# Optimization experiments

Hardware: AMD Instinct MI355X
Metric: run time of the kernel (lower is better)

The kernel has to match this reference:

```python
import jax, jax.numpy as jnp
import numpy as np

B, N, K, D = 256, 64, 12, 128


def setup_inputs() -> dict:
    key = jax.random.key(0)
    ks = jax.random.split(key, 12)
    s = 1.0 / np.sqrt(D)
    inp = {
        "nodes_hidden": jax.random.normal(ks[0], (B, N, D), jnp.float32),
        "neighbors_hidden": jax.random.normal(ks[1], (B, N, K, D), jnp.float32),
        # binary neighbor-validity mask (float, as in the torch code)
        "mask": (jax.random.uniform(ks[2], (B, N, K)) < 0.7).astype(jnp.float32),
        "Wq": jax.random.uniform(ks[3], (D, D), jnp.float32, -s, s),
        "bq": jax.random.uniform(ks[4], (D,), jnp.float32, -s, s),
        "Wk": jax.random.uniform(ks[5], (D, D), jnp.float32, -s, s),
        "bk": jax.random.uniform(ks[6], (D,), jnp.float32, -s, s),
        "Wv": jax.random.uniform(ks[7], (D, D), jnp.float32, -s, s),
        "bv": jax.random.uniform(ks[8], (D,), jnp.float32, -s, s),
        # W_att: Linear(2D -> 1); split into the query half and key half of its weight
        "wa_q": jax.random.uniform(ks[9], (D,), jnp.float32, -s, s),
        "wa_k": jax.random.uniform(ks[10], (D,), jnp.float32, -s, s),
        "ba": jax.random.uniform(ks[11], (), jnp.float32, -s, s),
    }
    return inp


def reference(nodes_hidden, neighbors_hidden, mask, Wq, bq, Wk, bk, Wv, bv, wa_q, wa_k, ba):
    # prepend the node itself to its neighbor list: [B,N,K+1,D]
    nh = jnp.concatenate([nodes_hidden[:, :, None, :], neighbors_hidden], axis=2)
    # prepend an always-valid slot to the mask: [B,N,K+1]
    m = jnp.concatenate([jnp.ones(mask.shape[:-1] + (1,), mask.dtype), mask], axis=-1)

    q = nodes_hidden @ Wq + bq            # [B,N,D]
    k = nh @ Wk + bk                      # [B,N,K+1,D]
    v = nh @ Wv + bv                      # [B,N,K+1,D]

    # W_att(cat([q,k])) == q.wa_q + k.wa_k + ba  (avoids materializing the 2D concat)
    sim = (q @ wa_q)[:, :, None] + k @ wa_k + ba   # [B,N,K+1]
    sim = jnp.where(sim >= 0, sim, 0.2 * sim)      # LeakyReLU(0.2)
    sim = jnp.exp(sim) * m                         # masked exp (matches torch exactly)
    attn = sim / (jnp.sum(sim, axis=-1, keepdims=True) + 1e-16)
    return jnp.einsum('bnk,bnkd->bnd', attn, v)    # [B,N,D]
```

## Files before the change

kernel.cpp:

```cpp
#include <hip/hip_runtime.h>


#define B_  256
#define N_  64
#define K_  12
#define D_  128
#define BN  (B_ * N_)

__global__ void prep_kernel(const float* __restrict__ Wq, const float* __restrict__ bq,
                            const float* __restrict__ Wk, const float* __restrict__ bk,
                            const float* __restrict__ wa_q, const float* __restrict__ wa_k,
                            float* __restrict__ ws) {
    int g = blockIdx.x;
    int l = threadIdx.x;
    const float* row;
    const float* wa;
    float* outp;
    if (g < 128)      { row = Wq + g * D_;         wa = wa_q; outp = ws + g; }
    else if (g < 256) { row = Wk + (g - 128) * D_; wa = wa_k; outp = ws + 128 + (g - 128); }
    else if (g == 256){ row = bq;                  wa = wa_q; outp = ws + 256; }
    else              { row = bk;                  wa = wa_k; outp = ws + 257; }

    float2 r = ((const float2*)row)[l];
    float2 w = ((const float2*)wa)[l];
    float p = r.x * w.x + r.y * w.y;
    #pragma unroll
    for (int m = 1; m < 64; m <<= 1) p += __shfl_xor(p, m, 64);
    if (l == 0) *outp = p;
}

#define HB_STRIDE 132
__global__ void __launch_bounds__(256)
fused_kernel(const float* __restrict__ nodes, const float* __restrict__ neigh,
             const float* __restrict__ mask, const float* __restrict__ ba_p,
             const float* __restrict__ ws, const float* __restrict__ Wv,
             const float* __restrict__ bv, float* __restrict__ out) {
    __shared__ float hb[32 * HB_STRIDE];
    __shared__ float scL[32];

    const int t    = threadIdx.x;
    const int wave = t >> 6;
    const int l    = t & 63;

    const float cq  = ws[256];
    const float ckb = ws[257];
    const float ba  = ba_p[0];
    const float cst = cq + ckb + ba;
    float2 wqe = ((const float2*)ws)[l];
    float2 wke = ((const float2*)(ws + 128))[l];

    for (int p = 0; p < 8; ++p) {
        const int lrow = wave * 8 + p;
        const int idx  = blockIdx.x * 32 + lrow;

        const float2* np = (const float2*)(nodes + (size_t)idx * D_);
        const float2* gp = (const float2*)(neigh + (size_t)idx * K_ * D_);

        float2 x[K_ + 1];
        x[0] = np[l];
        #pragma unroll
        for (int j = 0; j < K_; ++j) x[j + 1] = gp[j * 64 + l];

        float mval = (l < K_) ? mask[(size_t)idx * K_ + l] : 0.0f;

        float pq = x[0].x * wqe.x + x[0].y * wqe.y;
        float pk[K_ + 1];
        #pragma unroll
        for (int j = 0; j <= K_; ++j) pk[j] = x[j].x * wke.x + x[j].y * wke.y;

        #pragma unroll
        for (int m = 1; m < 64; m <<= 1) {
            pq += __shfl_xor(pq, m, 64);
            #pragma unroll
            for (int j = 0; j <= K_; ++j) pk[j] += __shfl_xor(pk[j], m, 64);
        }

        const float base = pq + cst;
        float e[K_ + 1];
        float S = 0.0f;
        #pragma unroll
        for (int j = 0; j <= K_; ++j) {
            float s = base + pk[j];
            s = (s >= 0.0f) ? s : 0.2f * s;
            float mj = (j == 0) ? 1.0f : __shfl(mval, j - 1, 64);
            e[j] = __expf(s) * mj;
            S += e[j];
        }
        const float inv = 1.0f / (S + 1e-16f);

        float h0 = 0.0f, h1 = 0.0f;
        #pragma unroll
        for (int j = 0; j <= K_; ++j) {
            float w = e[j] * inv;
            h0 += w * x[j].x;
            h1 += w * x[j].y;
        }

        *(float2*)(hb + lrow * HB_STRIDE + 2 * l) = make_float2(h0, h1);
        if (l == 0) scL[lrow] = S * inv;
    }
    __syncthreads();

    const int rg = t >> 5;
    const int cg = t & 31;
    const int row0 = blockIdx.x * 32;
    const float4* wv4 = (const float4*)Wv;

    float acc[4][4];
    #pragma unroll
    for (int i = 0; i < 4; ++i)
        #pragma unroll
        for (int c = 0; c < 4; ++c) acc[i][c] = 0.0f;

    #pragma unroll 8
    for (int k = 0; k < D_; ++k) {
        float4 b = wv4[k * 32 + cg];
        #pragma unroll
        for (int i = 0; i < 4; ++i) {
            float a = hb[(rg * 4 + i) * HB_STRIDE + k];
            acc[i][0] += a * b.x;
            acc[i][1] += a * b.y;
            acc[i][2] += a * b.z;
            acc[i][3] += a * b.w;
        }
    }

    float4 bvv = ((const float4*)bv)[cg];
    #pragma unroll
    for (int i = 0; i < 4; ++i) {
        float s = scL[rg * 4 + i];
        float4 o;
        o.x = acc[i][0] + bvv.x * s;
        o.y = acc[i][1] + bvv.y * s;
        o.z = acc[i][2] + bvv.z * s;
        o.w = acc[i][3] + bvv.w * s;
        *(float4*)(out + (size_t)(row0 + rg * 4 + i) * D_ + cg * 4) = o;
    }
}

extern "C" void kernel_launch(void* const* d_in, const int* in_sizes, int n_in,
                              void* d_out, int out_size, void* d_ws, size_t ws_size,
                              hipStream_t stream) {
    const float* nodes = (const float*)d_in[0];
    const float* neigh = (const float*)d_in[1];
    const float* mask  = (const float*)d_in[2];
    const float* Wq    = (const float*)d_in[3];
    const float* bq    = (const float*)d_in[4];
    const float* Wk    = (const float*)d_in[5];
    const float* bk    = (const float*)d_in[6];
    const float* Wv    = (const float*)d_in[7];
    const float* bv    = (const float*)d_in[8];
    const float* wa_q  = (const float*)d_in[9];
    const float* wa_k  = (const float*)d_in[10];
    const float* ba    = (const float*)d_in[11];
    float* out = (float*)d_out;
    float* ws  = (float*)d_ws;

    prep_kernel<<<258, 64, 0, stream>>>(Wq, bq, Wk, bk, wa_q, wa_k, ws);
    fused_kernel<<<BN / 32, 256, 0, stream>>>(nodes, neigh, mask, ba, ws, Wv, bv, out);
}
```

Before: 187.5 us.

## Fold weight-projection prep into fused kernel and shrink rows per block

Removes the separate prep kernel launch and has every block recompute the Wq·wa_q and Wk·wa_k projections and the bias constant in shared memory. The rows per block drop from 32 to 8, which quadruples the grid to 2048 blocks. The Wv matmul epilogue becomes one row per 32-thread group. This saves a launch and adds parallelism. In exchange each block redundantly reads 128 KB of Wq/Wk, and Wv reuse per block is lower.

```diff
diff --git a/kernel.cpp b/kernel.cpp
--- a/kernel.cpp
+++ b/kernel.cpp
@@ -6,52 +6,60 @@
 #define K_  12
 #define D_  128
 #define BN  (B_ * N_)
+#define ROWS 8
+#define NBLK (BN / ROWS)
+#define HB_STRIDE 132
 
-__global__ void prep_kernel(const float* __restrict__ Wq, const float* __restrict__ bq,
-                            const float* __restrict__ Wk, const float* __restrict__ bk,
-                            const float* __restrict__ wa_q, const float* __restrict__ wa_k,
-                            float* __restrict__ ws) {
-    int g = blockIdx.x;
-    int l = threadIdx.x;
-    const float* row;
-    const float* wa;
-    float* outp;
-    if (g < 128)      { row = Wq + g * D_;         wa = wa_q; outp = ws + g; }
-    else if (g < 256) { row = Wk + (g - 128) * D_; wa = wa_k; outp = ws + 128 + (g - 128); }
-    else if (g == 256){ row = bq;                  wa = wa_q; outp = ws + 256; }
-    else              { row = bk;                  wa = wa_k; outp = ws + 257; }
-
-    float2 r = ((const float2*)row)[l];
-    float2 w = ((const float2*)wa)[l];
-    float p = r.x * w.x + r.y * w.y;
-    #pragma unroll
-    for (int m = 1; m < 64; m <<= 1) p += __shfl_xor(p, m, 64);
-    if (l == 0) *outp = p;
-}
-
-#define HB_STRIDE 132
 __global__ void __launch_bounds__(256)
 fused_kernel(const float* __restrict__ nodes, const float* __restrict__ neigh,
-             const float* __restrict__ mask, const float* __restrict__ ba_p,
-             const float* __restrict__ ws, const float* __restrict__ Wv,
-             const float* __restrict__ bv, float* __restrict__ out) {
-    __shared__ float hb[32 * HB_STRIDE];
-    __shared__ float scL[32];
+             const float* __restrict__ mask,
+             const float* __restrict__ Wq, const float* __restrict__ bq,
+             const float* __restrict__ Wk, const float* __restrict__ bk,
+             const float* __restrict__ Wv, const float* __restrict__ bv,
+             const float* __restrict__ wa_q, const float* __restrict__ wa_k,
+             const float* __restrict__ ba_p, float* __restrict__ out) {
+    __shared__ float weff[256];
+    __shared__ float hb[ROWS * HB_STRIDE];
+    __shared__ float scL[ROWS];
+    __shared__ float cstS;
 
     const int t    = threadIdx.x;
     const int wave = t >> 6;
     const int l    = t & 63;
 
-    const float cq  = ws[256];
-    const float ckb = ws[257];
-    const float ba  = ba_p[0];
-    const float cst = cq + ckb + ba;
-    float2 wqe = ((const float2*)ws)[l];
-    float2 wke = ((const float2*)(ws + 128))[l];
+    {
+        const float*  wrow = (t < 128) ? (Wq + (size_t)t * D_) : (Wk + (size_t)(t - 128) * D_);
+        const float*  wa   = (t < 128) ? wa_q : wa_k;
+        const float4* wr4  = (const float4*)wrow;
+        const float4* wa4  = (const float4*)wa;
+        float acc = 0.0f;
+        #pragma unroll
+        for (int k = 0; k < 32; ++k) {
+            float4 a = wr4[k], b = wa4[k];
+            acc += a.x * b.x + a.y * b.y + a.z * b.z + a.w * b.w;
+        }
+        weff[t] = acc;
+    }
+    if (wave == 0) {
+        float2 q2  = ((const float2*)bq)[l];
+        float2 k2  = ((const float2*)bk)[l];
+        float2 aq2 = ((const float2*)wa_q)[l];
+        float2 ak2 = ((const float2*)wa_k)[l];
+        float c = q2.x * aq2.x + q2.y * aq2.y + k2.x * ak2.x + k2.y * ak2.y;
+        #pragma unroll
+        for (int m = 1; m < 64; m <<= 1) c += __shfl_xor(c, m, 64);
+        if (l == 0) cstS = c + ba_p[0];
+    }
+    __syncthreads();
 
-    for (int p = 0; p < 8; ++p) {
-        const int lrow = wave * 8 + p;
-        const int idx  = blockIdx.x * 32 + lrow;
+    const float cst = cstS;
+    const float2 wqe = ((const float2*)weff)[l];
+    const float2 wke = ((const float2*)(weff + 128))[l];
+
+    #pragma unroll
+    for (int p = 0; p < 2; ++p) {
+        const int lrow = wave * 2 + p;
+        const int idx  = blockIdx.x * ROWS + lrow;
 
         const float2* np = (const float2*)(nodes + (size_t)idx * D_);
         const float2* gp = (const float2*)(neigh + (size_t)idx * K_ * D_);
@@ -101,41 +109,30 @@
     }
     __syncthreads();
 
-    const int rg = t >> 5;
-    const int cg = t & 31;
-    const int row0 = blockIdx.x * 32;
+    const int row  = t >> 5;
+    const int cg   = t & 31;
+    const int row0 = blockIdx.x * ROWS;
     const float4* wv4 = (const float4*)Wv;
 
-    float acc[4][4];
-    #pragma unroll
-    for (int i = 0; i < 4; ++i)
-        #pragma unroll
-        for (int c = 0; c < 4; ++c) acc[i][c] = 0.0f;
-
+    float4 acc = make_float4(0.f, 0.f, 0.f, 0.f);
     #pragma unroll 8
     for (int k = 0; k < D_; ++k) {
         float4 b = wv4[k * 32 + cg];
-        #pragma unroll
-        for (int i = 0; i < 4; ++i) {
-            float a = hb[(rg * 4 + i) * HB_STRIDE + k];
-            acc[i][0] += a * b.x;
-            acc[i][1] += a * b.y;
-            acc[i][2] += a * b.z;
-            acc[i][3] += a * b.w;
-        }
+        float  a = hb[row * HB_STRIDE + k];
+        acc.x += a * b.x;
+        acc.y += a * b.y;
+        acc.z += a * b.z;
+        acc.w += a * b.w;
     }
 
     float4 bvv = ((const float4*)bv)[cg];
-    #pragma unroll
-    for (int i = 0; i < 4; ++i) {
-        float s = scL[rg * 4 + i];
-        float4 o;
-        o.x = acc[i][0] + bvv.x * s;
-        o.y = acc[i][1] + bvv.y * s;
-        o.z = acc[i][2] + bvv.z * s;
-        o.w = acc[i][3] + bvv.w * s;
-        *(float4*)(out + (size_t)(row0 + rg * 4 + i) * D_ + cg * 4) = o;
-    }
+    float  s   = scL[row];
+    float4 o;
+    o.x = acc.x + bvv.x * s;
+    o.y = acc.y + bvv.y * s;
+    o.z = acc.z + bvv.z * s;
+    o.w = acc.w + bvv.w * s;
+    *(float4*)(out + (size_t)(row0 + row) * D_ + cg * 4) = o;
 }
 
 extern "C" void kernel_launch(void* const* d_in, const int* in_sizes, int n_in,
@@ -154,8 +151,7 @@
     const float* wa_k  = (const float*)d_in[10];
     const float* ba    = (const float*)d_in[11];
     float* out = (float*)d_out;
-    float* ws  = (float*)d_ws;
 
-    prep_kernel<<<258, 64, 0, stream>>>(Wq, bq, Wk, bk, wa_q, wa_k, ws);
-    fused_kernel<<<BN / 32, 256, 0, stream>>>(nodes, neigh, mask, ba, ws, Wv, bv, out);
+    fused_kernel<<<NBLK, 256, 0, stream>>>(nodes, neigh, mask, Wq, bq, Wk, bk,
+                                           Wv, bv, wa_q, wa_k, ba, out);
 }
```

After: 224.8 us. 1.2x slower.
